# Performance work log

Hardware: AMD Instinct MI355X
Metric: run time of the kernel (lower is better)

The kernel has to match this reference:

```python
import jax, jax.numpy as jnp
import numpy as np

E, H, I = 8, 2048, 768  # num_experts, hidden_size, moe_intermediate_size
B, S = 4, 1024


def setup_inputs() -> dict:
    key = jax.random.key(0)
    k1, k2, k3, k4, k5 = jax.random.split(key, 5)
    hidden_states = jax.random.normal(k1, (B, S, H), dtype=jnp.float32)
    routing_weights = jax.random.uniform(k2, (B * S, E), dtype=jnp.float32)
    router_indices = jax.random.randint(k3, (B * S, 2), 0, E)
    gate_up_proj = jax.random.normal(k4, (E, H, 2 * I), dtype=jnp.float32) * 0.02
    down_proj = jax.random.normal(k5, (E, I, H), dtype=jnp.float32) * 0.02
    return {
        "hidden_states": hidden_states,
        "routing_weights": routing_weights,
        "router_indices": router_indices,
        "gate_up_proj": gate_up_proj,
        "down_proj": down_proj,
    }


def reference(hidden_states, routing_weights, router_indices, gate_up_proj, down_proj):
    b, s, h = hidden_states.shape
    x = hidden_states.reshape(-1, h)  # [T, H], T = B*S
    # dense all-experts: every token through every expert
    gate_up = jnp.einsum("th,ehd->etd", x, gate_up_proj)  # [E, T, 2I]
    gate, up = jnp.split(gate_up, 2, axis=-1)
    inter = up * jax.nn.silu(gate)  # [E, T, I]
    out = jnp.einsum("eti,eih->eth", inter, down_proj)  # [E, T, H]
    rw = routing_weights.T.reshape(out.shape[0], b, s)  # [E, B, S]
    out = out.reshape(out.shape[0], b, s, h) * rw[..., None]
    return out.sum(axis=0)  # [B, S, H]
```

## Files before the change

### kernel.cpp

```cpp
#include <hip/hip_runtime.h>
#include <cstdint>
#include <cstddef>

#define NE 8
#define NH 2048
#define NI 768
#define NT 4096
#define NK2 6144

typedef __bf16 bf16x8 __attribute__((ext_vector_type(8)));
typedef float f32x4 __attribute__((ext_vector_type(4)));
typedef unsigned short u16x8 __attribute__((ext_vector_type(8)));

__device__ __forceinline__ unsigned short f2bf(float f) {
  unsigned int u = __builtin_bit_cast(unsigned int, f);
  u += 0x7fffu + ((u >> 16) & 1u);
  return (unsigned short)(u >> 16);
}

__device__ __forceinline__ void gload_lds16(const void* g, void* s) {
  __builtin_amdgcn_global_load_lds(
      (const __attribute__((address_space(1))) unsigned int*)g,
      (__attribute__((address_space(3))) unsigned int*)s, 16, 0, 0);
}

__global__ __launch_bounds__(256) void k_cvt(const float* __restrict__ in,
                                             unsigned short* __restrict__ out,
                                             long n) {
  long i = ((long)blockIdx.x * blockDim.x + threadIdx.x) * 8;
  if (i >= n) return;
  float4 f0 = *reinterpret_cast<const float4*>(in + i);
  float4 f1 = *reinterpret_cast<const float4*>(in + i + 4);
  u16x8 o;
  o[0] = f2bf(f0.x); o[1] = f2bf(f0.y); o[2] = f2bf(f0.z); o[3] = f2bf(f0.w);
  o[4] = f2bf(f1.x); o[5] = f2bf(f1.y); o[6] = f2bf(f1.z); o[7] = f2bf(f1.w);
  *reinterpret_cast<u16x8*>(out + i) = o;
}

__global__ __launch_bounds__(256) void k_transpose_cvt(
    const float* __restrict__ in, unsigned short* __restrict__ out,
    int R, int C, long inBS, long outBS, int outCS, int mode) {
  __shared__ float tile[32][33];
  const int b = blockIdx.z;
  const int r0 = blockIdx.y * 32, c0 = blockIdx.x * 32;
  const int tx = threadIdx.x, ty = threadIdx.y;
  const float* ib = in + (long)b * inBS;
#pragma unroll
  for (int d = 0; d < 4; d++)
    tile[ty + d * 8][tx] = ib[(long)(r0 + ty + d * 8) * C + c0 + tx];
  __syncthreads();
#pragma unroll
  for (int d = 0; d < 4; d++) {
    int c = c0 + ty + d * 8;
    int r = r0 + tx;
    int orow;
    if (mode == 1) {
      int z = (c >= NI) ? 1 : 0;
      int cc = c - z * NI;
      orow = ((cc >> 4) << 5) + (z << 4) + (cc & 15);
    } else {
      orow = c;
    }
    out[(long)b * outBS + (long)orow * outCS + r] = f2bf(tile[tx][ty + d * 8]);
  }
}


__global__ __launch_bounds__(512, 2) void k_gemm1(
    const unsigned short* __restrict__ Xb,
    const unsigned short* __restrict__ W1t,
    const float* __restrict__ rw,
    unsigned short* __restrict__ inter) {
  __shared__ unsigned short ldsA[2][16384];
  __shared__ unsigned short ldsB[2][16384];

  const int e = blockIdx.z;
  const int t0 = blockIdx.y * 256;
  const int bn = blockIdx.x;
  const int tid = threadIdx.x;
  const int lane = tid & 63, wave = tid >> 6;
  const int wr = wave >> 2, wc = wave & 3;
  const int fr = lane & 15, fq = lane >> 4;
  const int nkt = NH / 64;

  const unsigned short* Bg = W1t + (size_t)e * (2 * NI) * NH;
  const int rih = tid >> 3, ck = tid & 7;
  const unsigned short* sA = Xb + (size_t)(t0 + rih) * NH + ((ck ^ (rih & 7)) << 3);
  const unsigned short* sB = Bg + (size_t)(bn * 256 + rih) * NH + ((ck ^ (rih & 7)) << 3);
  const int dst = tid * 8;

#define STG1(C) do { \
    const int cc_ = (C); \
    unsigned short* da_ = &ldsA[cc_ & 1][dst]; \
    unsigned short* db_ = &ldsB[cc_ & 1][dst]; \
    const size_t ko_ = (size_t)cc_ * 64; \
    _Pragma("unroll") \
    for (int q = 0; q < 4; ++q) { \
      gload_lds16(sA + ko_ + (size_t)q * (64 * NH), da_ + q * 4096); \
      gload_lds16(sB + ko_ + (size_t)q * (64 * NH), db_ + q * 4096); \
    } \
  } while (0)

  f32x4 acc[8][4];
#pragma unroll
  for (int i = 0; i < 8; ++i)
#pragma unroll
    for (int j = 0; j < 4; ++j) acc[i][j] = (f32x4){0.f, 0.f, 0.f, 0.f};

  const int swz = fr & 7;
  int aoff[8], boff[4];
#pragma unroll
  for (int i = 0; i < 8; ++i)
    aoff[i] = ((i >> 2) * 128 + wr * 64 + (i & 3) * 16 + fr) * 64 + ((fq ^ swz) << 3);
#pragma unroll
  for (int j = 0; j < 4; ++j)
    boff[j] = ((j >> 1) * 128 + wc * 32 + (j & 1) * 16 + fr) * 64 + ((fq ^ swz) << 3);
  const int dk = ((((4 + fq) ^ swz) - (fq ^ swz)) << 3);

  STG1(0);
  STG1(1);

  for (int kt = 0; kt < nkt; ++kt) {
    const int cur = kt & 1;
    const int nx = (kt + 1 < nkt) ? kt + 1 : nkt - 1;
    STG1(nx);
    asm volatile("s_waitcnt vmcnt(8)" ::: "memory");
    __builtin_amdgcn_sched_barrier(0);
    __builtin_amdgcn_s_barrier();
    __builtin_amdgcn_sched_barrier(0);
    {
      bf16x8 af[8], bf[4];
#pragma unroll
      for (int i = 0; i < 8; ++i)
        af[i] = *reinterpret_cast<const bf16x8*>(&ldsA[cur][aoff[i]]);
#pragma unroll
      for (int j = 0; j < 4; ++j)
        bf[j] = *reinterpret_cast<const bf16x8*>(&ldsB[cur][boff[j]]);
      __builtin_amdgcn_s_setprio(1);
#pragma unroll
      for (int i = 0; i < 8; ++i)
#pragma unroll
        for (int j = 0; j < 4; ++j)
          acc[i][j] = __builtin_amdgcn_mfma_f32_16x16x32_bf16(af[i], bf[j], acc[i][j], 0, 0, 0);
      __builtin_amdgcn_s_setprio(0);
    }
    {
      bf16x8 af[8], bf[4];
#pragma unroll
      for (int i = 0; i < 8; ++i)
        af[i] = *reinterpret_cast<const bf16x8*>(&ldsA[cur][aoff[i] + dk]);
#pragma unroll
      for (int j = 0; j < 4; ++j)
        bf[j] = *reinterpret_cast<const bf16x8*>(&ldsB[cur][boff[j] + dk]);
      __builtin_amdgcn_sched_barrier(0);
      __builtin_amdgcn_s_barrier();
      __builtin_amdgcn_sched_barrier(0);
      __builtin_amdgcn_s_setprio(1);
#pragma unroll
      for (int i = 0; i < 8; ++i)
#pragma unroll
        for (int j = 0; j < 4; ++j)
          acc[i][j] = __builtin_amdgcn_mfma_f32_16x16x32_bf16(af[i], bf[j], acc[i][j], 0, 0, 0);
      __builtin_amdgcn_s_setprio(0);
    }
  }
  asm volatile("s_waitcnt vmcnt(0)" ::: "memory");
#undef STG1

#pragma unroll
  for (int i = 0; i < 8; ++i) {
    const int trow = t0 + (i >> 2) * 128 + wr * 64 + (i & 3) * 16 + fq * 4;
#pragma unroll
    for (int r = 0; r < 4; ++r) {
      const int t = trow + r;
      const float rwv = rw[(size_t)t * NE + e];
#pragma unroll
      for (int p = 0; p < 2; ++p) {
        float g = acc[i][2 * p][r];
        float u = acc[i][2 * p + 1][r];
        float s = g / (1.f + __expf(-g));
        const int col = bn * 128 + (p * 4 + wc) * 16 + fr;
        inter[(size_t)t * NK2 + e * NI + col] = f2bf(rwv * u * s);
      }
    }
  }
}

__global__ __launch_bounds__(512, 2) void k_gemm2(
    const unsigned short* __restrict__ inter,
    const unsigned short* __restrict__ W2t,
    float* __restrict__ out) {
  __shared__ unsigned short ldsA[2][16384];
  __shared__ unsigned short ldsB[2][8192];

  const int t0 = blockIdx.y * 256;
  const int h0 = blockIdx.x * 128;
  const int tid = threadIdx.x;
  const int lane = tid & 63, wave = tid >> 6;
  const int wr = wave >> 1, wc = wave & 1;
  const int fr = lane & 15, fq = lane >> 4;
  const int nkt = NK2 / 64;

  const int rih = tid >> 3, ck = tid & 7;
  const unsigned short* sA = inter + (size_t)(t0 + rih) * NK2 + ((ck ^ (rih & 7)) << 3);
  const unsigned short* sB = W2t + (size_t)(h0 + rih) * NK2 + ((ck ^ (rih & 7)) << 3);
  const int dst = tid * 8;

#define STG2(C) do { \
    const int cc_ = (C); \
    unsigned short* da_ = &ldsA[cc_ & 1][dst]; \
    unsigned short* db_ = &ldsB[cc_ & 1][dst]; \
    const size_t ko_ = (size_t)cc_ * 64; \
    _Pragma("unroll") \
    for (int q = 0; q < 4; ++q) \
      gload_lds16(sA + ko_ + (size_t)q * (64 * NK2), da_ + q * 4096); \
    _Pragma("unroll") \
    for (int q = 0; q < 2; ++q) \
      gload_lds16(sB + ko_ + (size_t)q * (64 * NK2), db_ + q * 4096); \
  } while (0)

  f32x4 acc[4][4];
#pragma unroll
  for (int i = 0; i < 4; ++i)
#pragma unroll
    for (int j = 0; j < 4; ++j) acc[i][j] = (f32x4){0.f, 0.f, 0.f, 0.f};

  const int swz = fr & 7;
  int aoff[4], boff[4];
#pragma unroll
  for (int i = 0; i < 4; ++i)
    aoff[i] = (wr * 64 + i * 16 + fr) * 64 + ((fq ^ swz) << 3);
#pragma unroll
  for (int j = 0; j < 4; ++j)
    boff[j] = (wc * 64 + j * 16 + fr) * 64 + ((fq ^ swz) << 3);
  const int dk = ((((4 + fq) ^ swz) - (fq ^ swz)) << 3);

  STG2(0);
  STG2(1);

  for (int kt = 0; kt < nkt; ++kt) {
    const int cur = kt & 1;
    const int nx = (kt + 1 < nkt) ? kt + 1 : nkt - 1;
    STG2(nx);
    asm volatile("s_waitcnt vmcnt(6)" ::: "memory");
    __builtin_amdgcn_sched_barrier(0);
    __builtin_amdgcn_s_barrier();
    __builtin_amdgcn_sched_barrier(0);
    {
      bf16x8 af[4], bf[4];
#pragma unroll
      for (int i = 0; i < 4; ++i)
        af[i] = *reinterpret_cast<const bf16x8*>(&ldsA[cur][aoff[i]]);
#pragma unroll
      for (int j = 0; j < 4; ++j)
        bf[j] = *reinterpret_cast<const bf16x8*>(&ldsB[cur][boff[j]]);
      __builtin_amdgcn_s_setprio(1);
#pragma unroll
      for (int i = 0; i < 4; ++i)
#pragma unroll
        for (int j = 0; j < 4; ++j)
          acc[i][j] = __builtin_amdgcn_mfma_f32_16x16x32_bf16(af[i], bf[j], acc[i][j], 0, 0, 0);
      __builtin_amdgcn_s_setprio(0);
    }
    {
      bf16x8 af[4], bf[4];
#pragma unroll
      for (int i = 0; i < 4; ++i)
        af[i] = *reinterpret_cast<const bf16x8*>(&ldsA[cur][aoff[i] + dk]);
#pragma unroll
      for (int j = 0; j < 4; ++j)
        bf[j] = *reinterpret_cast<const bf16x8*>(&ldsB[cur][boff[j] + dk]);
      __builtin_amdgcn_sched_barrier(0);
      __builtin_amdgcn_s_barrier();
      __builtin_amdgcn_sched_barrier(0);
      __builtin_amdgcn_s_setprio(1);
#pragma unroll
      for (int i = 0; i < 4; ++i)
#pragma unroll
        for (int j = 0; j < 4; ++j)
          acc[i][j] = __builtin_amdgcn_mfma_f32_16x16x32_bf16(af[i], bf[j], acc[i][j], 0, 0, 0);
      __builtin_amdgcn_s_setprio(0);
    }
  }
  asm volatile("s_waitcnt vmcnt(0)" ::: "memory");
#undef STG2

  const int rowBase = t0 + wr * 64 + fq * 4;
#pragma unroll
  for (int i = 0; i < 4; ++i)
#pragma unroll
    for (int j = 0; j < 4; ++j)
#pragma unroll
      for (int r = 0; r < 4; ++r)
        out[(size_t)(rowBase + i * 16 + r) * NH + h0 + wc * 64 + j * 16 + fr] =
            acc[i][j][r];
}

extern "C" void kernel_launch(void* const* d_in, const int* in_sizes, int n_in,
                              void* d_out, int out_size, void* d_ws, size_t ws_size,
                              hipStream_t stream) {
  const float* x = (const float*)d_in[0];
  const float* rw = (const float*)d_in[1];
  const float* w1 = (const float*)d_in[3];
  const float* w2 = (const float*)d_in[4];
  float* out = (float*)d_out;

  char* ws = (char*)d_ws;
  unsigned short* Xb = (unsigned short*)ws;
  unsigned short* W1t = (unsigned short*)(ws + 16777216);
  unsigned short* W2t = (unsigned short*)(ws + 16777216 + 50331648);
  unsigned short* inter = (unsigned short*)(ws + 16777216 + 50331648 + 25165824);

  k_cvt<<<dim3((NT * NH) / (256 * 8)), dim3(256), 0, stream>>>(x, Xb, (long)NT * NH);
  k_transpose_cvt<<<dim3((2 * NI) / 32, NH / 32, NE), dim3(32, 8), 0, stream>>>(
      w1, W1t, NH, 2 * NI, (long)NH * 2 * NI, (long)2 * NI * NH, NH, 1);
  k_transpose_cvt<<<dim3(NH / 32, NI / 32, NE), dim3(32, 8), 0, stream>>>(
      w2, W2t, NI, NH, (long)NI * NH, (long)NI, NK2, 0);
  k_gemm1<<<dim3((2 * NI) / 256, NT / 256, NE), dim3(512), 0, stream>>>(Xb, W1t, rw, inter);
  k_gemm2<<<dim3(NH / 128, NT / 256), dim3(512), 0, stream>>>(inter, W2t, out);
}
```

Before: 366.9 us.

## Restructure gemm1 main loop into four-phase interleaved load/MFMA schedule

Splits each K-tile of the first GEMM into four quadrant phases. Each phase loads a slice of the LDS fragments, issues half of the next tile's global-to-LDS loads, then runs its MFMAs between barriers, so memory traffic overlaps with matrix work at finer grain. The prologue now stages only tile 0 instead of two tiles, and launch bounds drop to one block per CU to free registers for the extra fragment buffers. This risks lower occupancy and more barriers per tile in exchange for tighter overlap.

```diff
diff --git a/kernel.cpp b/kernel.cpp
--- a/kernel.cpp
+++ b/kernel.cpp
@@ -66,7 +66,7 @@
 }
 
 
-__global__ __launch_bounds__(512, 2) void k_gemm1(
+__global__ __launch_bounds__(512, 1) void k_gemm1(
     const unsigned short* __restrict__ Xb,
     const unsigned short* __restrict__ W1t,
     const float* __restrict__ rw,
@@ -89,17 +89,28 @@
   const unsigned short* sB = Bg + (size_t)(bn * 256 + rih) * NH + ((ck ^ (rih & 7)) << 3);
   const int dst = tid * 8;
 
-#define STG1(C) do { \
-    const int cc_ = (C); \
+#define STG_H0(C) do { \
+    const int cc_ = (C); const size_t ko_ = (size_t)cc_ * 64; \
     unsigned short* da_ = &ldsA[cc_ & 1][dst]; \
     unsigned short* db_ = &ldsB[cc_ & 1][dst]; \
-    const size_t ko_ = (size_t)cc_ * 64; \
-    _Pragma("unroll") \
-    for (int q = 0; q < 4; ++q) { \
-      gload_lds16(sA + ko_ + (size_t)q * (64 * NH), da_ + q * 4096); \
-      gload_lds16(sB + ko_ + (size_t)q * (64 * NH), db_ + q * 4096); \
-    } \
+    gload_lds16(sB + ko_, db_); \
+    gload_lds16(sB + ko_ + (size_t)(64 * NH), db_ + 4096); \
+    gload_lds16(sA + ko_, da_); \
+    gload_lds16(sA + ko_ + (size_t)(64 * NH), da_ + 4096); \
   } while (0)
+#define STG_H1(C) do { \
+    const int cc_ = (C); const size_t ko_ = (size_t)cc_ * 64; \
+    unsigned short* da_ = &ldsA[cc_ & 1][dst]; \
+    unsigned short* db_ = &ldsB[cc_ & 1][dst]; \
+    gload_lds16(sB + ko_ + (size_t)2 * (64 * NH), db_ + 8192); \
+    gload_lds16(sB + ko_ + (size_t)3 * (64 * NH), db_ + 12288); \
+    gload_lds16(sA + ko_ + (size_t)2 * (64 * NH), da_ + 8192); \
+    gload_lds16(sA + ko_ + (size_t)3 * (64 * NH), da_ + 12288); \
+  } while (0)
+#define WAITV4 asm volatile("s_waitcnt vmcnt(4)" ::: "memory")
+#define BAR do { __builtin_amdgcn_sched_barrier(0); \
+                 __builtin_amdgcn_s_barrier(); \
+                 __builtin_amdgcn_sched_barrier(0); } while (0)
 
   f32x4 acc[8][4];
 #pragma unroll
@@ -117,55 +128,96 @@
     boff[j] = ((j >> 1) * 128 + wc * 32 + (j & 1) * 16 + fr) * 64 + ((fq ^ swz) << 3);
   const int dk = ((((4 + fq) ^ swz) - (fq ^ swz)) << 3);
 
-  STG1(0);
-  STG1(1);
+  STG_H0(0);
+  STG_H1(0);
+  WAITV4;
+  BAR;
 
   for (int kt = 0; kt < nkt; ++kt) {
     const int cur = kt & 1;
     const int nx = (kt + 1 < nkt) ? kt + 1 : nkt - 1;
-    STG1(nx);
-    asm volatile("s_waitcnt vmcnt(8)" ::: "memory");
-    __builtin_amdgcn_sched_barrier(0);
-    __builtin_amdgcn_s_barrier();
-    __builtin_amdgcn_sched_barrier(0);
-    {
-      bf16x8 af[8], bf[4];
-#pragma unroll
-      for (int i = 0; i < 8; ++i)
-        af[i] = *reinterpret_cast<const bf16x8*>(&ldsA[cur][aoff[i]]);
-#pragma unroll
-      for (int j = 0; j < 4; ++j)
-        bf[j] = *reinterpret_cast<const bf16x8*>(&ldsB[cur][boff[j]]);
-      __builtin_amdgcn_s_setprio(1);
-#pragma unroll
-      for (int i = 0; i < 8; ++i)
-#pragma unroll
-        for (int j = 0; j < 4; ++j)
-          acc[i][j] = __builtin_amdgcn_mfma_f32_16x16x32_bf16(af[i], bf[j], acc[i][j], 0, 0, 0);
-      __builtin_amdgcn_s_setprio(0);
-    }
-    {
-      bf16x8 af[8], bf[4];
-#pragma unroll
-      for (int i = 0; i < 8; ++i)
-        af[i] = *reinterpret_cast<const bf16x8*>(&ldsA[cur][aoff[i] + dk]);
-#pragma unroll
-      for (int j = 0; j < 4; ++j)
-        bf[j] = *reinterpret_cast<const bf16x8*>(&ldsB[cur][boff[j] + dk]);
-      __builtin_amdgcn_sched_barrier(0);
-      __builtin_amdgcn_s_barrier();
-      __builtin_amdgcn_sched_barrier(0);
-      __builtin_amdgcn_s_setprio(1);
-#pragma unroll
-      for (int i = 0; i < 8; ++i)
-#pragma unroll
-        for (int j = 0; j < 4; ++j)
-          acc[i][j] = __builtin_amdgcn_mfma_f32_16x16x32_bf16(af[i], bf[j], acc[i][j], 0, 0, 0);
-      __builtin_amdgcn_s_setprio(0);
-    }
+    const unsigned short* lA = ldsA[cur];
+    const unsigned short* lB = ldsB[cur];
+    bf16x8 af0[4][2], af1[4][2], bf0[2][2], bf1[2][2];
+
+#pragma unroll
+    for (int m = 0; m < 4; ++m) {
+      af0[m][0] = *reinterpret_cast<const bf16x8*>(lA + aoff[m]);
+      af0[m][1] = *reinterpret_cast<const bf16x8*>(lA + aoff[m] + dk);
+    }
+#pragma unroll
+    for (int jj = 0; jj < 2; ++jj) {
+      bf0[jj][0] = *reinterpret_cast<const bf16x8*>(lB + boff[jj]);
+      bf0[jj][1] = *reinterpret_cast<const bf16x8*>(lB + boff[jj] + dk);
+    }
+    STG_H0(nx);
+    WAITV4;
+    BAR;
+    __builtin_amdgcn_s_setprio(1);
+#pragma unroll
+    for (int kk = 0; kk < 2; ++kk)
+#pragma unroll
+      for (int m = 0; m < 4; ++m)
+#pragma unroll
+        for (int jj = 0; jj < 2; ++jj)
+          acc[m][jj] = __builtin_amdgcn_mfma_f32_16x16x32_bf16(af0[m][kk], bf0[jj][kk], acc[m][jj], 0, 0, 0);
+    __builtin_amdgcn_s_setprio(0);
+
+#pragma unroll
+    for (int jj = 0; jj < 2; ++jj) {
+      bf1[jj][0] = *reinterpret_cast<const bf16x8*>(lB + boff[2 + jj]);
+      bf1[jj][1] = *reinterpret_cast<const bf16x8*>(lB + boff[2 + jj] + dk);
+    }
+    STG_H1(nx);
+    BAR;
+    __builtin_amdgcn_s_setprio(1);
+#pragma unroll
+    for (int kk = 0; kk < 2; ++kk)
+#pragma unroll
+      for (int m = 0; m < 4; ++m)
+#pragma unroll
+        for (int jj = 0; jj < 2; ++jj)
+          acc[m][2 + jj] = __builtin_amdgcn_mfma_f32_16x16x32_bf16(af0[m][kk], bf1[jj][kk], acc[m][2 + jj], 0, 0, 0);
+    __builtin_amdgcn_s_setprio(0);
+
+#pragma unroll
+    for (int m = 0; m < 4; ++m) {
+      af1[m][0] = *reinterpret_cast<const bf16x8*>(lA + aoff[4 + m]);
+      af1[m][1] = *reinterpret_cast<const bf16x8*>(lA + aoff[4 + m] + dk);
+    }
+    BAR;
+    __builtin_amdgcn_s_setprio(1);
+#pragma unroll
+    for (int kk = 0; kk < 2; ++kk)
+#pragma unroll
+      for (int m = 0; m < 4; ++m)
+#pragma unroll
+        for (int jj = 0; jj < 2; ++jj)
+          acc[4 + m][2 + jj] = __builtin_amdgcn_mfma_f32_16x16x32_bf16(af1[m][kk], bf1[jj][kk], acc[4 + m][2 + jj], 0, 0, 0);
+    __builtin_amdgcn_s_setprio(0);
+
+#pragma unroll
+    for (int jj = 0; jj < 2; ++jj) {
+      bf0[jj][0] = *reinterpret_cast<const bf16x8*>(lB + boff[jj]);
+      bf0[jj][1] = *reinterpret_cast<const bf16x8*>(lB + boff[jj] + dk);
+    }
+    WAITV4;
+    BAR;
+    __builtin_amdgcn_s_setprio(1);
+#pragma unroll
+    for (int kk = 0; kk < 2; ++kk)
+#pragma unroll
+      for (int m = 0; m < 4; ++m)
+#pragma unroll
+        for (int jj = 0; jj < 2; ++jj)
+          acc[4 + m][jj] = __builtin_amdgcn_mfma_f32_16x16x32_bf16(af1[m][kk], bf0[jj][kk], acc[4 + m][jj], 0, 0, 0);
+    __builtin_amdgcn_s_setprio(0);
   }
   asm volatile("s_waitcnt vmcnt(0)" ::: "memory");
-#undef STG1
+#undef STG_H0
+#undef STG_H1
+#undef WAITV4
+#undef BAR
 
 #pragma unroll
   for (int i = 0; i < 8; ++i) {
```

Measured after the change: 366.7 us. About the same (-0.0%).

## Restructure GEMM mainloops to load full K-tile fragments before issuing next prefetch

Applied to the files above, without the earlier changes.

Both GEMM kernels replace the two-ahead prefetch pipeline with a simpler scheme. Each iteration reads both K-halves of the fragments from LDS, issues the global->LDS load for the next tile into the other buffer, runs all MFMAs, then waits for vmcnt(0) and barriers. Launch bounds drop from 2 to 1 block per CU, which frees registers for the larger fragment arrays but may cut occupancy. The setprio hints and the partial vmcnt waits are removed, so memory latency may be hidden less well.

```diff
diff --git a/kernel.cpp b/kernel.cpp
--- a/kernel.cpp
+++ b/kernel.cpp
@@ -66,7 +66,7 @@
 }
 
 
-__global__ __launch_bounds__(512, 2) void k_gemm1(
+__global__ __launch_bounds__(512, 1) void k_gemm1(
     const unsigned short* __restrict__ Xb,
     const unsigned short* __restrict__ W1t,
     const float* __restrict__ rw,
@@ -90,10 +90,9 @@
   const int dst = tid * 8;
 
 #define STG1(C) do { \
-    const int cc_ = (C); \
+    const int cc_ = (C); const size_t ko_ = (size_t)cc_ * 64; \
     unsigned short* da_ = &ldsA[cc_ & 1][dst]; \
     unsigned short* db_ = &ldsB[cc_ & 1][dst]; \
-    const size_t ko_ = (size_t)cc_ * 64; \
     _Pragma("unroll") \
     for (int q = 0; q < 4; ++q) { \
       gload_lds16(sA + ko_ + (size_t)q * (64 * NH), da_ + q * 4096); \
@@ -118,53 +117,39 @@
   const int dk = ((((4 + fq) ^ swz) - (fq ^ swz)) << 3);
 
   STG1(0);
-  STG1(1);
+  asm volatile("s_waitcnt vmcnt(0)" ::: "memory");
+  asm volatile("s_barrier" ::: "memory");
 
   for (int kt = 0; kt < nkt; ++kt) {
     const int cur = kt & 1;
-    const int nx = (kt + 1 < nkt) ? kt + 1 : nkt - 1;
-    STG1(nx);
-    asm volatile("s_waitcnt vmcnt(8)" ::: "memory");
-    __builtin_amdgcn_sched_barrier(0);
-    __builtin_amdgcn_s_barrier();
-    __builtin_amdgcn_sched_barrier(0);
-    {
-      bf16x8 af[8], bf[4];
-#pragma unroll
-      for (int i = 0; i < 8; ++i)
-        af[i] = *reinterpret_cast<const bf16x8*>(&ldsA[cur][aoff[i]]);
-#pragma unroll
-      for (int j = 0; j < 4; ++j)
-        bf[j] = *reinterpret_cast<const bf16x8*>(&ldsB[cur][boff[j]]);
-      __builtin_amdgcn_s_setprio(1);
-#pragma unroll
-      for (int i = 0; i < 8; ++i)
+    const unsigned short* lA = ldsA[cur];
+    const unsigned short* lB = ldsB[cur];
+
+    bf16x8 af[8][2], bf[4][2];
+#pragma unroll
+    for (int m = 0; m < 8; ++m) {
+      af[m][0] = *reinterpret_cast<const bf16x8*>(lA + aoff[m]);
+      af[m][1] = *reinterpret_cast<const bf16x8*>(lA + aoff[m] + dk);
+    }
+#pragma unroll
+    for (int j = 0; j < 4; ++j) {
+      bf[j][0] = *reinterpret_cast<const bf16x8*>(lB + boff[j]);
+      bf[j][1] = *reinterpret_cast<const bf16x8*>(lB + boff[j] + dk);
+    }
+
+    if (kt + 1 < nkt) STG1(kt + 1);
+
+#pragma unroll
+    for (int kk = 0; kk < 2; ++kk)
+#pragma unroll
+      for (int m = 0; m < 8; ++m)
 #pragma unroll
         for (int j = 0; j < 4; ++j)
-          acc[i][j] = __builtin_amdgcn_mfma_f32_16x16x32_bf16(af[i], bf[j], acc[i][j], 0, 0, 0);
-      __builtin_amdgcn_s_setprio(0);
-    }
-    {
-      bf16x8 af[8], bf[4];
-#pragma unroll
-      for (int i = 0; i < 8; ++i)
-        af[i] = *reinterpret_cast<const bf16x8*>(&ldsA[cur][aoff[i] + dk]);
-#pragma unroll
-      for (int j = 0; j < 4; ++j)
-        bf[j] = *reinterpret_cast<const bf16x8*>(&ldsB[cur][boff[j] + dk]);
-      __builtin_amdgcn_sched_barrier(0);
-      __builtin_amdgcn_s_barrier();
-      __builtin_amdgcn_sched_barrier(0);
-      __builtin_amdgcn_s_setprio(1);
-#pragma unroll
-      for (int i = 0; i < 8; ++i)
-#pragma unroll
-        for (int j = 0; j < 4; ++j)
-          acc[i][j] = __builtin_amdgcn_mfma_f32_16x16x32_bf16(af[i], bf[j], acc[i][j], 0, 0, 0);
-      __builtin_amdgcn_s_setprio(0);
-    }
-  }
-  asm volatile("s_waitcnt vmcnt(0)" ::: "memory");
+          acc[m][j] = __builtin_amdgcn_mfma_f32_16x16x32_bf16(af[m][kk], bf[j][kk], acc[m][j], 0, 0, 0);
+
+    asm volatile("s_waitcnt vmcnt(0)" ::: "memory");
+    asm volatile("s_barrier" ::: "memory");
+  }
 #undef STG1
 
 #pragma unroll
@@ -186,7 +171,7 @@
   }
 }
 
-__global__ __launch_bounds__(512, 2) void k_gemm2(
+__global__ __launch_bounds__(512, 1) void k_gemm2(
     const unsigned short* __restrict__ inter,
     const unsigned short* __restrict__ W2t,
     float* __restrict__ out) {
@@ -236,53 +221,39 @@
   const int dk = ((((4 + fq) ^ swz) - (fq ^ swz)) << 3);
 
   STG2(0);
-  STG2(1);
+  asm volatile("s_waitcnt vmcnt(0)" ::: "memory");
+  asm volatile("s_barrier" ::: "memory");
 
   for (int kt = 0; kt < nkt; ++kt) {
     const int cur = kt & 1;
-    const int nx = (kt + 1 < nkt) ? kt + 1 : nkt - 1;
-    STG2(nx);
-    asm volatile("s_waitcnt vmcnt(6)" ::: "memory");
-    __builtin_amdgcn_sched_barrier(0);
-    __builtin_amdgcn_s_barrier();
-    __builtin_amdgcn_sched_barrier(0);
-    {
-      bf16x8 af[4], bf[4];
+    const unsigned short* lA = ldsA[cur];
+    const unsigned short* lB = ldsB[cur];
+
+    bf16x8 af[4][2], bf[4][2];
+#pragma unroll
+    for (int i = 0; i < 4; ++i) {
+      af[i][0] = *reinterpret_cast<const bf16x8*>(lA + aoff[i]);
+      af[i][1] = *reinterpret_cast<const bf16x8*>(lA + aoff[i] + dk);
+    }
+#pragma unroll
+    for (int j = 0; j < 4; ++j) {
+      bf[j][0] = *reinterpret_cast<const bf16x8*>(lB + boff[j]);
+      bf[j][1] = *reinterpret_cast<const bf16x8*>(lB + boff[j] + dk);
+    }
+
+    if (kt + 1 < nkt) STG2(kt + 1);
+
+#pragma unroll
+    for (int kk = 0; kk < 2; ++kk)
 #pragma unroll
       for (int i = 0; i < 4; ++i)
-        af[i] = *reinterpret_cast<const bf16x8*>(&ldsA[cur][aoff[i]]);
-#pragma unroll
-      for (int j = 0; j < 4; ++j)
-        bf[j] = *reinterpret_cast<const bf16x8*>(&ldsB[cur][boff[j]]);
-      __builtin_amdgcn_s_setprio(1);
-#pragma unroll
-      for (int i = 0; i < 4; ++i)
 #pragma unroll
         for (int j = 0; j < 4; ++j)
-          acc[i][j] = __builtin_amdgcn_mfma_f32_16x16x32_bf16(af[i], bf[j], acc[i][j], 0, 0, 0);
-      __builtin_amdgcn_s_setprio(0);
-    }
-    {
-      bf16x8 af[4], bf[4];
-#pragma unroll
-      for (int i = 0; i < 4; ++i)
-        af[i] = *reinterpret_cast<const bf16x8*>(&ldsA[cur][aoff[i] + dk]);
-#pragma unroll
-      for (int j = 0; j < 4; ++j)
-        bf[j] = *reinterpret_cast<const bf16x8*>(&ldsB[cur][boff[j] + dk]);
-      __builtin_amdgcn_sched_barrier(0);
-      __builtin_amdgcn_s_barrier();
-      __builtin_amdgcn_sched_barrier(0);
-      __builtin_amdgcn_s_setprio(1);
-#pragma unroll
-      for (int i = 0; i < 4; ++i)
-#pragma unroll
-        for (int j = 0; j < 4; ++j)
-          acc[i][j] = __builtin_amdgcn_mfma_f32_16x16x32_bf16(af[i], bf[j], acc[i][j], 0, 0, 0);
-      __builtin_amdgcn_s_setprio(0);
-    }
-  }
-  asm volatile("s_waitcnt vmcnt(0)" ::: "memory");
+          acc[i][j] = __builtin_amdgcn_mfma_f32_16x16x32_bf16(af[i][kk], bf[j][kk], acc[i][j], 0, 0, 0);
+
+    asm volatile("s_waitcnt vmcnt(0)" ::: "memory");
+    asm volatile("s_barrier" ::: "memory");
+  }
 #undef STG2
 
   const int rowBase = t0 + wr * 64 + fq * 4;
```

After: 362.1 us. About the same (-1.3%).
